# Kernel tuning notes

Hardware: AMD Instinct MI355X
Metric: run time of the kernel (lower is better)

## Reference

```python
import jax, jax.numpy as jnp
import numpy as np

N = 2048          # batch
T = 50            # max_num_visit
CODES = 40        # codes per visit
VOCAB = 527       # max_tokens for CategoryEncoding
MH = VOCAB - 1    # 526 after dropping column 0
AUX = 10          # aux_info feature dim
E = 256           # config.embedding_dim (LSTM units)


def setup_inputs() -> dict:
    key = jax.random.key(0)
    ks = jax.random.split(key, 10)
    code = jax.random.randint(ks[0], (N, T, CODES), 0, VOCAB, dtype=jnp.int32)
    aux_info = jax.random.normal(ks[1], (N, T, AUX), jnp.float32)
    length = jax.random.randint(ks[2], (N,), 1, T + 1, dtype=jnp.int32)

    def glorot(k, shape):
        fan = shape[0]
        return jax.random.normal(k, shape, jnp.float32) * (1.0 / np.sqrt(fan))

    W_lin = glorot(ks[3], (MH + AUX, E)); b_lin = jnp.zeros((E,), jnp.float32)
    K_lstm = glorot(ks[4], (E, 4 * E))
    R_lstm = glorot(ks[5], (E, 4 * E))
    b_lstm = jnp.zeros((4 * E,), jnp.float32)
    W0 = glorot(ks[6], (E, 256)); b0 = jnp.zeros((256,), jnp.float32)
    W1 = glorot(ks[7], (256, 256)); b1 = jnp.zeros((256,), jnp.float32)
    return dict(code=code, aux_info=aux_info, length=length, is_training=0,
                W_lin=W_lin, b_lin=b_lin, K_lstm=K_lstm, R_lstm=R_lstm,
                b_lstm=b_lstm, W0=W0, b0=b0, W1=W1, b1=b1)


def _multi_hot(code):
    # CategoryEncoding binary mode: presence indicator over vocab, drop col 0
    flat = code.reshape(N * T, CODES)
    mh = jnp.zeros((N * T, VOCAB), jnp.float32)
    mh = mh.at[jnp.arange(N * T)[:, None], flat].set(1.0)
    return mh[:, 1:].reshape(N, T, MH)


def _lstm(x, K, R, b):
    # Keras LSTM, gate order [i, f, g(c), o]; inference (dropout off)
    xz = jnp.einsum('nte,eh->nth', x, K) + b          # [N,T,4E]
    xz = jnp.transpose(xz, (1, 0, 2))                  # [T,N,4E]

    def step(carry, zt):
        h, c = carry
        z = zt + h @ R
        i, f, g, o = jnp.split(z, 4, axis=-1)
        c = jax.nn.sigmoid(f) * c + jax.nn.sigmoid(i) * jnp.tanh(g)
        h = jax.nn.sigmoid(o) * jnp.tanh(c)
        return (h, c), h

    h0 = jnp.zeros((N, E), jnp.float32)
    (_, _), hs = jax.lax.scan(step, (h0, h0), xz)
    return jnp.transpose(hs, (1, 0, 2))                # [N,T,E]


def reference(code, aux_info, length, is_training,
              W_lin, b_lin, K_lstm, R_lstm, b_lstm, W0, b0, W1, b1):
    mh = _multi_hot(code)                              # [N,T,526]
    x = jax.nn.relu(jnp.concatenate([mh, aux_info], axis=-1) @ W_lin + b_lin)
    h = _lstm(x, K_lstm, R_lstm, b_lstm)               # [N,T,E]
    x_last = h[jnp.arange(N), length - 1]              # gather_nd: last valid step
    fv = jax.nn.relu(x_last @ W0 + b0) @ W1 + b1
    fv = fv / jnp.sqrt(jnp.sum(fv ** 2, axis=-1, keepdims=True))
    return fv
```

## Files before the change

kernel.cpp:

```cpp
#include <hip/hip_runtime.h>
#include <hip/hip_bf16.h>
#include <math.h>
#include <stdint.h>

#define N_BATCH 2048
#define T_STEPS 50
#define NCODES  40
#define MH      526
#define AUXD    10
#define WLROWS  536
#define E_DIM   256
#define G_DIM   1024
#define TCHUNK  10
#define MBLK    64
#define NFUSED  (TCHUNK * 32)

typedef __attribute__((ext_vector_type(8))) short short8;
typedef __attribute__((ext_vector_type(4))) short short4v;
typedef __attribute__((ext_vector_type(4))) float f32x4;
typedef __attribute__((ext_vector_type(4))) int   i32x4;

__device__ __forceinline__ short f2bf(float f) {
    __hip_bfloat16 h = __float2bfloat16(f);
    return *reinterpret_cast<short*>(&h);
}
__device__ __forceinline__ float bf2f(unsigned short u) {
    return __uint_as_float(((unsigned int)u) << 16);
}
__device__ __forceinline__ float sigf(float x) {
    return 1.f / (1.f + __expf(-x));
}
__device__ __forceinline__ float tanhfast(float x) {
    return 2.f / (1.f + __expf(-2.f * x)) - 1.f;
}

__global__ __launch_bounds__(256) void k_zero(int* __restrict__ cnt)
{
    const int i = blockIdx.x * 256 + threadIdx.x;
    if (i < 3 * 64 * 32) cnt[i] = 0;
}

__global__ __launch_bounds__(256) void k_prep_wcoop(
    const float* __restrict__ R, short* __restrict__ Wcoop)
{
    const int gid  = blockIdx.x * 256 + threadIdx.x;
    const int fg   = gid >> 6, lane = gid & 63;
    const int p    = lane >> 4, lr = lane & 15;
    const int kk   = fg & 7;
    const int g    = (fg >> 3) & 3;
    const int w    = (fg >> 5) & 3;
    const int cs   = fg >> 7;
    const int n    = g * 256 + cs * 64 + w * 16 + lr;
    short* dst = Wcoop + (size_t)fg * 512 + lane * 8;
    #pragma unroll
    for (int j = 0; j < 8; ++j)
        dst[j] = f2bf(R[(size_t)(kk * 32 + p * 8 + j) * G_DIM + n]);
}

__global__ __launch_bounds__(256) void k_prep_wfk(
    const float* __restrict__ K, short* __restrict__ WfK)
{
    const int gid  = blockIdx.x * 256 + threadIdx.x;
    const int fg   = gid >> 6, lane = gid & 63;
    const int p    = lane >> 4, lr = lane & 15;
    const int kb   = fg >> 6;
    const int cb   = (fg >> 3) & 7;
    const int w    = fg & 7;
    const int n    = w * 128 + cb * 16 + lr;
    short* dst = WfK + (size_t)fg * 512 + lane * 8;
    #pragma unroll
    for (int j = 0; j < 8; ++j)
        dst[j] = f2bf(K[(size_t)(kb * 32 + p * 8 + j) * G_DIM + n]);
}

__global__ __launch_bounds__(256) void k_prep_wfl(
    const float* __restrict__ W_lin, short* __restrict__ WfL)
{
    const int gid  = blockIdx.x * 256 + threadIdx.x;
    const int fg   = gid >> 6, lane = gid & 63;
    const int p    = lane >> 4, lr = lane & 15;
    const int kk   = fg >> 4;
    const int cb   = (fg >> 3) & 1;
    const int w    = fg & 7;
    const int n    = w * 32 + cb * 16 + lr;
    short* dst = WfL + (size_t)fg * 512 + lane * 8;
    #pragma unroll
    for (int j = 0; j < 8; ++j) {
        const int k = kk * 32 + p * 8 + j;
        dst[j] = (k < WLROWS) ? f2bf(W_lin[(size_t)k * E_DIM + n]) : (short)0;
    }
}

__global__ __launch_bounds__(512, 1) void k_fused(
    const int* __restrict__ code, const float* __restrict__ aux,
    const short* __restrict__ WfL, const float* __restrict__ b_lin,
    const short* __restrict__ WfK, short* __restrict__ xzp, int t0f)
{
    const int tid  = threadIdx.x;
    const int w    = tid >> 6;
    const int lane = tid & 63;
    const int lr   = lane & 15;
    const int p    = lane >> 4;
    const int fid  = blockIdx.x;
    const int tl   = fid >> 5;
    const int ngg  = fid & 31;
    const int n0   = ngg * MBLK;
    const int t    = t0f + tl;
    const int ph8  = (fid >> 3) & 7;
    const int ph17 = (fid >> 3) % 17;

    __shared__ __align__(16) short oh[MBLK][552];
    __shared__ __align__(16) short xs[MBLK][264];

    for (int i = tid; i < (MBLK * 552) / 8; i += 512)
        ((int4*)&oh[0][0])[i] = (int4){0, 0, 0, 0};
    __syncthreads();

    for (int i = tid; i < MBLK * NCODES; i += 512) {
        const int r = i / NCODES;
        const int j = i - r * NCODES;
        const int c = code[((size_t)(n0 + r) * T_STEPS + t) * NCODES + j];
        if (c > 0) ((unsigned short*)&oh[0][0])[r * 552 + (c - 1)] = 0x3F80;
    }
    for (int i = tid; i < MBLK * AUXD; i += 512) {
        const int r = i / AUXD;
        const int a = i - r * AUXD;
        oh[r][MH + a] = f2bf(aux[((size_t)(n0 + r) * T_STEPS + t) * AUXD + a]);
    }
    __syncthreads();

    const short* wfl_thr = WfL + (size_t)w * 512 + lane * 8;
    const short* wfk_thr = WfK + (size_t)w * 512 + lane * 8;

    {
        f32x4 acc[4][2];
        #pragma unroll
        for (int rb = 0; rb < 4; ++rb)
            #pragma unroll
            for (int cb = 0; cb < 2; ++cb)
                acc[rb][cb] = (f32x4){0.f, 0.f, 0.f, 0.f};

        for (int kk = 0; kk < 17; ++kk) {
            int kx = kk + ph17; if (kx >= 17) kx -= 17;
            short8 a[4];
            #pragma unroll
            for (int rb = 0; rb < 4; ++rb)
                a[rb] = *(const short8*)&oh[rb * 16 + lr][kx * 32 + p * 8];
            #pragma unroll
            for (int cb = 0; cb < 2; ++cb) {
                short8 bf = *(const short8*)(wfl_thr + (size_t)(kx * 2 + cb) * 4096);
                #pragma unroll
                for (int rb = 0; rb < 4; ++rb)
                    acc[rb][cb] = __builtin_amdgcn_mfma_f32_16x16x32_bf16(
                        a[rb], bf, acc[rb][cb], 0, 0, 0);
            }
        }
        float bias[2];
        #pragma unroll
        for (int cb = 0; cb < 2; ++cb) bias[cb] = b_lin[w * 32 + cb * 16 + lr];
        #pragma unroll
        for (int rb = 0; rb < 4; ++rb)
            #pragma unroll
            for (int cb = 0; cb < 2; ++cb)
                #pragma unroll
                for (int rr = 0; rr < 4; ++rr)
                    xs[rb * 16 + p * 4 + rr][w * 32 + cb * 16 + lr] =
                        f2bf(fmaxf(acc[rb][cb][rr] + bias[cb], 0.f));
        __syncthreads();
    }

    #pragma unroll
    for (int half = 0; half < 2; ++half) {
        f32x4 acc[4][4];
        #pragma unroll
        for (int rb = 0; rb < 4; ++rb)
            #pragma unroll
            for (int c4 = 0; c4 < 4; ++c4)
                acc[rb][c4] = (f32x4){0.f, 0.f, 0.f, 0.f};

        for (int kb = 0; kb < 8; ++kb) {
            const int kx = (kb + ph8) & 7;
            short8 a[4];
            #pragma unroll
            for (int rb = 0; rb < 4; ++rb)
                a[rb] = *(const short8*)&xs[rb * 16 + lr][kx * 32 + p * 8];
            #pragma unroll
            for (int c4 = 0; c4 < 4; ++c4) {
                const int cb = half * 4 + c4;
                short8 bf = *(const short8*)(wfk_thr + (size_t)(kx * 8 + cb) * 4096);
                #pragma unroll
                for (int rb = 0; rb < 4; ++rb)
                    acc[rb][c4] = __builtin_amdgcn_mfma_f32_16x16x32_bf16(
                        a[rb], bf, acc[rb][c4], 0, 0, 0);
            }
        }
        #pragma unroll
        for (int rb = 0; rb < 4; ++rb) {
            const int rgg = ngg * 4 + rb;
            #pragma unroll
            for (int c4 = 0; c4 < 4; ++c4) {
                const int cb = half * 4 + c4;
                const int c0 = w * 128 + cb * 16;
                const int g  = c0 >> 8;
                const int wp = (c0 >> 5) & 7;
                const int eb = (c0 >> 4) & 1;
                const int j8 = eb * 4 + g;
                short4v v;
                #pragma unroll
                for (int rr = 0; rr < 4; ++rr) v[rr] = f2bf(acc[rb][c4][rr]);
                *(short4v*)(xzp +
                    (((size_t)rgg * TCHUNK + tl) * 64 + wp * 8 + j8) * 256 +
                    lane * 4) = v;
            }
        }
    }
}

__global__ __launch_bounds__(256, 1) void k_rcoop(
    const short* __restrict__ xz0, const short* __restrict__ xz1,
    const int* __restrict__ length,
    const short* __restrict__ Wcoop, const float* __restrict__ b,
    short* __restrict__ h_buf, float* __restrict__ c_state,
    float* __restrict__ xlast, int* __restrict__ flags,
    int t0, int nsteps)
{
    const int tid  = threadIdx.x;
    const int w    = tid >> 6;
    const int lane = tid & 63;
    const int lr   = lane & 15;
    const int p    = lane >> 4;
    const int cs   = blockIdx.x >> 6;
    const int rg   = blockIdx.x & 63;
    const int r0   = rg * 32;
    const int e    = cs * 64 + w * 16 + lr;

    __shared__ __align__(16) short h_o[32][64];
    __shared__ int s_len[32];
    if (tid < 32) s_len[tid] = length[r0 + tid];

    short8 bw[4][8];
    {
        const short* wb = Wcoop + ((size_t)((cs * 4 + w) * 4)) * 8 * 512 + lane * 8;
        #pragma unroll
        for (int g = 0; g < 4; ++g)
            #pragma unroll
            for (int kk = 0; kk < 8; ++kk)
                bw[g][kk] = *(const short8*)(wb + (size_t)(g * 8 + kk) * 512);
    }

    float bias[4];
    #pragma unroll
    for (int g = 0; g < 4; ++g) bias[g] = b[g * 256 + e];

    float creg[2][4];
    if (t0 == 0) {
        #pragma unroll
        for (int rf = 0; rf < 2; ++rf)
            #pragma unroll
            for (int rr = 0; rr < 4; ++rr) creg[rf][rr] = 0.f;
    } else {
        #pragma unroll
        for (int rf = 0; rf < 2; ++rf)
            #pragma unroll
            for (int rr = 0; rr < 4; ++rr)
                creg[rf][rr] = c_state[(size_t)(r0 + rf * 16 + p * 4 + rr) * E_DIM + e];
    }
    __syncthreads();

    int len_r[2][4];
    #pragma unroll
    for (int rf = 0; rf < 2; ++rf)
        #pragma unroll
        for (int rr = 0; rr < 4; ++rr)
            len_r[rf][rr] = s_len[rf * 16 + p * 4 + rr];

    const uint64_t slot_addr = (uint64_t)(uintptr_t)(flags + rg * 32 + cs);
    const uint64_t line_addr = (uint64_t)(uintptr_t)(flags + rg * 32);
    int bcnt = 0;

#define PEERS_BARRIER()                                                        \
    do {                                                                       \
        ++bcnt;                                                                \
        __syncthreads();               \
        if (tid == 0) {                                                        \
            asm volatile("global_store_dword %0, %1, off sc0 sc1"              \
                         :: "v"(slot_addr), "v"(bcnt) : "memory");             \
            i32x4 fv;                                                          \
            do {                                                               \
                asm volatile("global_load_dwordx4 %0, %1, off sc0 sc1\n\t"     \
                             "s_waitcnt vmcnt(0)"                              \
                             : "=v"(fv) : "v"(line_addr) : "memory");          \
            } while (fv[0] < bcnt || fv[1] < bcnt ||                           \
                     fv[2] < bcnt || fv[3] < bcnt);                            \
        }                                                                      \
        __syncthreads();                                                       \
    } while (0)

    if (t0 == 0) {
        const i32x4 z4 = {0, 0, 0, 0};
        const int row = tid >> 3, seg = tid & 7;
        const uint64_t dst = (uint64_t)(uintptr_t)(h_buf +
            (size_t)(r0 + row) * E_DIM + cs * 64 + seg * 8);
        asm volatile("global_store_dwordx4 %0, %1, off sc0 sc1"
                     :: "v"(dst), "v"(z4) : "memory");
        PEERS_BARRIER();
    }

    const short* hb0 = h_buf;
    const short* hb1 = h_buf + (size_t)N_BATCH * E_DIM;
    const size_t coloff = (size_t)((cs * 2 + (w >> 1)) * 8 + (w & 1) * 4) * 256 +
                          lane * 4;
    const size_t rowoff0 = (size_t)(2 * rg + 0) * TCHUNK * 16384;
    const size_t rowoff1 = (size_t)(2 * rg + 1) * TCHUNK * 16384;

#define XZ_BASE(T, RFOFF)                                                      \
    ((((((T) / TCHUNK) & 1) ? xz1 : xz0)) + (RFOFF) +                          \
     (size_t)((T) % TCHUNK) * 16384 + coloff)

    short4v xv[2][4];
    {
        const short* b0p = XZ_BASE(t0, rowoff0);
        const short* b1p = XZ_BASE(t0, rowoff1);
        #pragma unroll
        for (int g = 0; g < 4; ++g) {
            xv[0][g] = *(const short4v*)(b0p + g * 256);
            xv[1][g] = *(const short4v*)(b1p + g * 256);
        }
    }

    for (int s = 0; s < nsteps; ++s) {
        const int t = t0 + s;
        const short* hb_r = (t & 1) ? hb1 : hb0;

        short8 a[2][8];
        #pragma unroll
        for (int rf = 0; rf < 2; ++rf) {
            const uint64_t base = (uint64_t)(uintptr_t)(hb_r +
                (size_t)(r0 + rf * 16 + lr) * E_DIM + p * 8);
            asm volatile(
                "global_load_dwordx4 %0, %8, off sc0 sc1\n\t"
                "global_load_dwordx4 %1, %8, off offset:64 sc0 sc1\n\t"
                "global_load_dwordx4 %2, %8, off offset:128 sc0 sc1\n\t"
                "global_load_dwordx4 %3, %8, off offset:192 sc0 sc1\n\t"
                "global_load_dwordx4 %4, %8, off offset:256 sc0 sc1\n\t"
                "global_load_dwordx4 %5, %8, off offset:320 sc0 sc1\n\t"
                "global_load_dwordx4 %6, %8, off offset:384 sc0 sc1\n\t"
                "global_load_dwordx4 %7, %8, off offset:448 sc0 sc1"
                : "=&v"(a[rf][0]), "=&v"(a[rf][1]), "=&v"(a[rf][2]), "=&v"(a[rf][3]),
                  "=&v"(a[rf][4]), "=&v"(a[rf][5]), "=&v"(a[rf][6]), "=&v"(a[rf][7])
                : "v"(base));
        }

        f32x4 acc[2][4];
        #pragma unroll
        for (int rf = 0; rf < 2; ++rf)
            #pragma unroll
            for (int g = 0; g < 4; ++g)
                #pragma unroll
                for (int rr = 0; rr < 4; ++rr)
                    acc[rf][g][rr] = bf2f((unsigned short)xv[rf][g][rr]);

        asm volatile("s_waitcnt vmcnt(0)" ::: "memory");
        __builtin_amdgcn_sched_barrier(0);

        #pragma unroll
        for (int kk = 0; kk < 8; ++kk)
            #pragma unroll
            for (int g = 0; g < 4; ++g)
                #pragma unroll
                for (int rf = 0; rf < 2; ++rf)
                    acc[rf][g] = __builtin_amdgcn_mfma_f32_16x16x32_bf16(
                        a[rf][kk], bw[g][kk], acc[rf][g], 0, 0, 0);

        if (s + 1 < nsteps) {
            const short* b0p = XZ_BASE(t + 1, rowoff0);
            const short* b1p = XZ_BASE(t + 1, rowoff1);
            #pragma unroll
            for (int g = 0; g < 4; ++g) {
                xv[0][g] = *(const short4v*)(b0p + g * 256);
                xv[1][g] = *(const short4v*)(b1p + g * 256);
            }
        }

        #pragma unroll
        for (int rf = 0; rf < 2; ++rf) {
            #pragma unroll
            for (int rr = 0; rr < 4; ++rr) {
                float zi = acc[rf][0][rr] + bias[0];
                float zf = acc[rf][1][rr] + bias[1];
                float zg = acc[rf][2][rr] + bias[2];
                float zo = acc[rf][3][rr] + bias[3];
                float ig = sigf(zi), fg = sigf(zf);
                float gg = tanhfast(zg), og = sigf(zo);
                float cc = fg * creg[rf][rr] + ig * gg;
                float hh = og * tanhfast(cc);
                creg[rf][rr] = cc;
                h_o[rf * 16 + p * 4 + rr][w * 16 + lr] = f2bf(hh);
                const int row = r0 + rf * 16 + p * 4 + rr;
                if (t == len_r[rf][rr] - 1)
                    xlast[(size_t)row * E_DIM + e] = hh;
            }
        }
        __syncthreads();

        {
            short* hb_w = (short*)(((t + 1) & 1) ? hb1 : hb0);
            const int row = tid >> 3, seg = tid & 7;
            i32x4 v = *(const i32x4*)&h_o[row][seg * 8];
            const uint64_t dst = (uint64_t)(uintptr_t)(hb_w +
                (size_t)(r0 + row) * E_DIM + cs * 64 + seg * 8);
            asm volatile("global_store_dwordx4 %0, %1, off sc0 sc1"
                         :: "v"(dst), "v"(v) : "memory");
        }

        if (s + 1 < nsteps) PEERS_BARRIER();
    }

    #pragma unroll
    for (int rf = 0; rf < 2; ++rf)
        #pragma unroll
        for (int rr = 0; rr < 4; ++rr)
            c_state[(size_t)(r0 + rf * 16 + p * 4 + rr) * E_DIM + e] = creg[rf][rr];
#undef PEERS_BARRIER
#undef XZ_BASE
}

__global__ __launch_bounds__(256) void k_head(
    const float* __restrict__ xlast,
    const float* __restrict__ W0, const float* __restrict__ b0,
    const float* __restrict__ W1, const float* __restrict__ b1,
    float* __restrict__ out)
{
    const int n = blockIdx.x;
    const int j = threadIdx.x;

    __shared__ __align__(16) float xsh[E_DIM];
    __shared__ __align__(16) float y0[E_DIM];
    __shared__ float part[4];

    xsh[j] = xlast[(size_t)n * E_DIM + j];
    __syncthreads();

    float acc = b0[j];
    for (int k4 = 0; k4 < E_DIM; k4 += 4) {
        float4 xv = *reinterpret_cast<const float4*>(&xsh[k4]);
        #pragma unroll
        for (int kk = 0; kk < 4; ++kk)
            acc += (&xv.x)[kk] * W0[(size_t)(k4 + kk) * E_DIM + j];
    }
    y0[j] = fmaxf(acc, 0.f);
    __syncthreads();

    acc = b1[j];
    for (int k4 = 0; k4 < E_DIM; k4 += 4) {
        float4 yv = *reinterpret_cast<const float4*>(&y0[k4]);
        #pragma unroll
        for (int kk = 0; kk < 4; ++kk)
            acc += (&yv.x)[kk] * W1[(size_t)(k4 + kk) * E_DIM + j];
    }

    float sq = acc * acc;
    #pragma unroll
    for (int off = 32; off > 0; off >>= 1)
        sq += __shfl_xor(sq, off, 64);
    if ((j & 63) == 0) part[j >> 6] = sq;
    __syncthreads();
    float total = part[0] + part[1] + part[2] + part[3];

    out[(size_t)n * E_DIM + j] = acc * rsqrtf(total);
}

extern "C" void kernel_launch(void* const* d_in, const int* in_sizes, int n_in,
                              void* d_out, int out_size, void* d_ws, size_t ws_size,
                              hipStream_t stream) {
    const int*   code   = (const int*)  d_in[0];
    const float* aux    = (const float*)d_in[1];
    const int*   length = (const int*)  d_in[2];
    const float* W_lin  = (const float*)d_in[4];
    const float* b_lin  = (const float*)d_in[5];
    const float* K      = (const float*)d_in[6];
    const float* R      = (const float*)d_in[7];
    const float* b      = (const float*)d_in[8];
    const float* W0     = (const float*)d_in[9];
    const float* b0     = (const float*)d_in[10];
    const float* W1     = (const float*)d_in[11];
    const float* b1     = (const float*)d_in[12];
    float* out = (float*)d_out;

    char* ws = (char*)d_ws;
    short* Wcoop   = (short*)(ws + 0);
    short* WfK     = (short*)(ws + 524288);
    short* WfL     = (short*)(ws + 1048576);
    float* xlast   = (float*)(ws + 1327104);
    float* c_state = (float*)(ws + 3424256);
    short* h_buf   = (short*)(ws + 5521408);
    int*   flags   = (int*)  (ws + 7618560);
    short* xzp0    = (short*)(ws + 7643136);
    short* xzp1    = (short*)(ws + 49586176);

    k_zero      <<<24,  256, 0, stream>>>(flags);
    k_prep_wcoop<<<128, 256, 0, stream>>>(R, Wcoop);
    k_prep_wfk  <<<128, 256, 0, stream>>>(K, WfK);
    k_prep_wfl  <<<68,  256, 0, stream>>>(W_lin, WfL);

    k_fused<<<NFUSED, 512, 0, stream>>>(code, aux, WfL, b_lin, WfK, xzp0, 0);
    k_fused<<<NFUSED, 512, 0, stream>>>(code, aux, WfL, b_lin, WfK, xzp1, 10);
    k_rcoop<<<256, 256, 0, stream>>>(xzp0, xzp1, length, Wcoop, b, h_buf,
                                     c_state, xlast, flags + 0 * 2048, 0, 20);
    k_fused<<<NFUSED, 512, 0, stream>>>(code, aux, WfL, b_lin, WfK, xzp0, 20);
    k_fused<<<NFUSED, 512, 0, stream>>>(code, aux, WfL, b_lin, WfK, xzp1, 30);
    k_rcoop<<<256, 256, 0, stream>>>(xzp0, xzp1, length, Wcoop, b, h_buf,
                                     c_state, xlast, flags + 1 * 2048, 20, 20);
    k_fused<<<NFUSED, 512, 0, stream>>>(code, aux, WfL, b_lin, WfK, xzp0, 40);
    k_rcoop<<<256, 256, 0, stream>>>(xzp0, xzp1, length, Wcoop, b, h_buf,
                                     c_state, xlast, flags + 2 * 2048, 40, 10);

    k_head<<<N_BATCH, 256, 0, stream>>>(xlast, W0, b0, W1, b1, out);
}
```

Measured before the change: 478.8 us.

## Process 64 batch rows per recurrent block and stage h through LDS

The recurrent LSTM kernel now gives each block 64 batch rows instead of 32, halving the grid from 256 to 128 blocks. Each block still holds the same register-resident slice of R, so each weight load is reused over twice as many rows. The previous h state is loaded cooperatively with coalesced loads, rearranged into the MFMA operand layout in shared memory, and then read from LDS, replacing per-lane strided global loads. The trade-off is half as many blocks in flight (fewer CUs busy), more serial MFMA and gate work per block per step, and extra LDS traffic plus a __syncthreads.

```diff
diff --git a/kernel.cpp b/kernel.cpp
--- a/kernel.cpp
+++ b/kernel.cpp
@@ -37,7 +37,7 @@
 __global__ __launch_bounds__(256) void k_zero(int* __restrict__ cnt)
 {
     const int i = blockIdx.x * 256 + threadIdx.x;
-    if (i < 3 * 64 * 32) cnt[i] = 0;
+    if (i < 3 * 32 * 32) cnt[i] = 0;
 }
 
 __global__ __launch_bounds__(256) void k_prep_wcoop(
@@ -229,14 +229,15 @@
     const int lane = tid & 63;
     const int lr   = lane & 15;
     const int p    = lane >> 4;
-    const int cs   = blockIdx.x >> 6;
-    const int rg   = blockIdx.x & 63;
-    const int r0   = rg * 32;
+    const int cs   = blockIdx.x >> 5;
+    const int rgp  = blockIdx.x & 31;
+    const int r0   = rgp * 64;
     const int e    = cs * 64 + w * 16 + lr;
 
-    __shared__ __align__(16) short h_o[32][64];
-    __shared__ int s_len[32];
-    if (tid < 32) s_len[tid] = length[r0 + tid];
+    __shared__ __align__(16) short h_f[2][2][8][512];
+    __shared__ __align__(16) short h_o[2][32][64];
+    __shared__ int s_len[64];
+    if (tid < 64) s_len[tid] = length[r0 + tid];
 
     short8 bw[4][8];
     {
@@ -252,30 +253,37 @@
     #pragma unroll
     for (int g = 0; g < 4; ++g) bias[g] = b[g * 256 + e];
 
-    float creg[2][4];
+    float creg[2][2][4];
     if (t0 == 0) {
         #pragma unroll
+        for (int rg = 0; rg < 2; ++rg)
+            #pragma unroll
+            for (int rf = 0; rf < 2; ++rf)
+                #pragma unroll
+                for (int rr = 0; rr < 4; ++rr) creg[rg][rf][rr] = 0.f;
+    } else {
+        #pragma unroll
+        for (int rg = 0; rg < 2; ++rg)
+            #pragma unroll
+            for (int rf = 0; rf < 2; ++rf)
+                #pragma unroll
+                for (int rr = 0; rr < 4; ++rr)
+                    creg[rg][rf][rr] = c_state[
+                        (size_t)(r0 + rg * 32 + rf * 16 + p * 4 + rr) * E_DIM + e];
+    }
+    __syncthreads();
+
+    int len_r[2][2][4];
+    #pragma unroll
+    for (int rg = 0; rg < 2; ++rg)
+        #pragma unroll
         for (int rf = 0; rf < 2; ++rf)
             #pragma unroll
-            for (int rr = 0; rr < 4; ++rr) creg[rf][rr] = 0.f;
-    } else {
-        #pragma unroll
-        for (int rf = 0; rf < 2; ++rf)
-            #pragma unroll
             for (int rr = 0; rr < 4; ++rr)
-                creg[rf][rr] = c_state[(size_t)(r0 + rf * 16 + p * 4 + rr) * E_DIM + e];
-    }
-    __syncthreads();
-
-    int len_r[2][4];
-    #pragma unroll
-    for (int rf = 0; rf < 2; ++rf)
-        #pragma unroll
-        for (int rr = 0; rr < 4; ++rr)
-            len_r[rf][rr] = s_len[rf * 16 + p * 4 + rr];
-
-    const uint64_t slot_addr = (uint64_t)(uintptr_t)(flags + rg * 32 + cs);
-    const uint64_t line_addr = (uint64_t)(uintptr_t)(flags + rg * 32);
+                len_r[rg][rf][rr] = s_len[rg * 32 + rf * 16 + p * 4 + rr];
+
+    const uint64_t slot_addr = (uint64_t)(uintptr_t)(flags + rgp * 32 + cs);
+    const uint64_t line_addr = (uint64_t)(uintptr_t)(flags + rgp * 32);
     int bcnt = 0;
 
 #define PEERS_BARRIER()                                                        \
@@ -298,11 +306,15 @@
 
     if (t0 == 0) {
         const i32x4 z4 = {0, 0, 0, 0};
-        const int row = tid >> 3, seg = tid & 7;
-        const uint64_t dst = (uint64_t)(uintptr_t)(h_buf +
-            (size_t)(r0 + row) * E_DIM + cs * 64 + seg * 8);
-        asm volatile("global_store_dwordx4 %0, %1, off sc0 sc1"
-                     :: "v"(dst), "v"(z4) : "memory");
+        #pragma unroll
+        for (int rep = 0; rep < 2; ++rep) {
+            const int idx = tid + rep * 256;
+            const int row = idx >> 3, seg = idx & 7;
+            const uint64_t dst = (uint64_t)(uintptr_t)(h_buf +
+                (size_t)(r0 + row) * E_DIM + cs * 64 + seg * 8);
+            asm volatile("global_store_dwordx4 %0, %1, off sc0 sc1"
+                         :: "v"(dst), "v"(z4) : "memory");
+        }
         PEERS_BARRIER();
     }
 
@@ -310,117 +322,141 @@
     const short* hb1 = h_buf + (size_t)N_BATCH * E_DIM;
     const size_t coloff = (size_t)((cs * 2 + (w >> 1)) * 8 + (w & 1) * 4) * 256 +
                           lane * 4;
-    const size_t rowoff0 = (size_t)(2 * rg + 0) * TCHUNK * 16384;
-    const size_t rowoff1 = (size_t)(2 * rg + 1) * TCHUNK * 16384;
+    size_t rowoff[2][2];
+    #pragma unroll
+    for (int rg = 0; rg < 2; ++rg)
+        #pragma unroll
+        for (int rf = 0; rf < 2; ++rf)
+            rowoff[rg][rf] = (size_t)(rgp * 4 + rg * 2 + rf) * TCHUNK * 16384;
 
 #define XZ_BASE(T, RFOFF)                                                      \
     ((((((T) / TCHUNK) & 1) ? xz1 : xz0)) + (RFOFF) +                          \
      (size_t)((T) % TCHUNK) * 16384 + coloff)
 
-    short4v xv[2][4];
-    {
-        const short* b0p = XZ_BASE(t0, rowoff0);
-        const short* b1p = XZ_BASE(t0, rowoff1);
-        #pragma unroll
-        for (int g = 0; g < 4; ++g) {
-            xv[0][g] = *(const short4v*)(b0p + g * 256);
-            xv[1][g] = *(const short4v*)(b1p + g * 256);
-        }
-    }
+    short4v xv[2][2][4];
+    #pragma unroll
+    for (int rg = 0; rg < 2; ++rg)
+        #pragma unroll
+        for (int rf = 0; rf < 2; ++rf) {
+            const short* bp = XZ_BASE(t0, rowoff[rg][rf]);
+            #pragma unroll
+            for (int g = 0; g < 4; ++g)
+                xv[rg][rf][g] = *(const short4v*)(bp + g * 256);
+        }
 
     for (int s = 0; s < nsteps; ++s) {
         const int t = t0 + s;
         const short* hb_r = (t & 1) ? hb1 : hb0;
 
-        short8 a[2][8];
-        #pragma unroll
-        for (int rf = 0; rf < 2; ++rf) {
-            const uint64_t base = (uint64_t)(uintptr_t)(hb_r +
-                (size_t)(r0 + rf * 16 + lr) * E_DIM + p * 8);
-            asm volatile(
-                "global_load_dwordx4 %0, %8, off sc0 sc1\n\t"
-                "global_load_dwordx4 %1, %8, off offset:64 sc0 sc1\n\t"
-                "global_load_dwordx4 %2, %8, off offset:128 sc0 sc1\n\t"
-                "global_load_dwordx4 %3, %8, off offset:192 sc0 sc1\n\t"
-                "global_load_dwordx4 %4, %8, off offset:256 sc0 sc1\n\t"
-                "global_load_dwordx4 %5, %8, off offset:320 sc0 sc1\n\t"
-                "global_load_dwordx4 %6, %8, off offset:384 sc0 sc1\n\t"
-                "global_load_dwordx4 %7, %8, off offset:448 sc0 sc1"
-                : "=&v"(a[rf][0]), "=&v"(a[rf][1]), "=&v"(a[rf][2]), "=&v"(a[rf][3]),
-                  "=&v"(a[rf][4]), "=&v"(a[rf][5]), "=&v"(a[rf][6]), "=&v"(a[rf][7])
-                : "v"(base));
-        }
-
-        f32x4 acc[2][4];
-        #pragma unroll
-        for (int rf = 0; rf < 2; ++rf)
-            #pragma unroll
-            for (int g = 0; g < 4; ++g)
-                #pragma unroll
-                for (int rr = 0; rr < 4; ++rr)
-                    acc[rf][g][rr] = bf2f((unsigned short)xv[rf][g][rr]);
-
-        asm volatile("s_waitcnt vmcnt(0)" ::: "memory");
-        __builtin_amdgcn_sched_barrier(0);
-
-        #pragma unroll
-        for (int kk = 0; kk < 8; ++kk)
-            #pragma unroll
-            for (int g = 0; g < 4; ++g)
-                #pragma unroll
-                for (int rf = 0; rf < 2; ++rf)
-                    acc[rf][g] = __builtin_amdgcn_mfma_f32_16x16x32_bf16(
-                        a[rf][kk], bw[g][kk], acc[rf][g], 0, 0, 0);
+        {
+            short8 ld[8];
+            int dof[8];
+            #pragma unroll
+            for (int it = 0; it < 8; ++it) {
+                const int idx = tid + it * 256;
+                const int rg  = idx >> 10;
+                const int rem = idx & 1023;
+                const int row = rem >> 5;
+                const int ch  = rem & 31;
+                const uint64_t src = (uint64_t)(uintptr_t)(hb_r +
+                    (size_t)(r0 + rg * 32 + row) * E_DIM + ch * 8);
+                asm volatile("global_load_dwordx4 %0, %1, off sc0 sc1"
+                             : "=&v"(ld[it]) : "v"(src) : "memory");
+                dof[it] = ((rg * 2 + (row >> 4)) * 8 + (ch >> 2)) * 512 +
+                          ((ch & 3) * 16 + (row & 15)) * 8;
+            }
+            asm volatile("s_waitcnt vmcnt(0)" ::: "memory");
+            #pragma unroll
+            for (int it = 0; it < 8; ++it)
+                *(short8*)(&h_f[0][0][0][0] + dof[it]) = ld[it];
+        }
+        __syncthreads();
+
+        #pragma unroll
+        for (int rg = 0; rg < 2; ++rg) {
+            f32x4 acc[2][4];
+            #pragma unroll
+            for (int rf = 0; rf < 2; ++rf)
+                #pragma unroll
+                for (int g = 0; g < 4; ++g)
+                    #pragma unroll
+                    for (int rr = 0; rr < 4; ++rr)
+                        acc[rf][g][rr] = bf2f((unsigned short)xv[rg][rf][g][rr]);
+
+            #pragma unroll
+            for (int kk = 0; kk < 8; ++kk) {
+                short8 a0 = *(const short8*)&h_f[rg][0][kk][lane * 8];
+                short8 a1 = *(const short8*)&h_f[rg][1][kk][lane * 8];
+                #pragma unroll
+                for (int g = 0; g < 4; ++g) {
+                    acc[0][g] = __builtin_amdgcn_mfma_f32_16x16x32_bf16(
+                        a0, bw[g][kk], acc[0][g], 0, 0, 0);
+                    acc[1][g] = __builtin_amdgcn_mfma_f32_16x16x32_bf16(
+                        a1, bw[g][kk], acc[1][g], 0, 0, 0);
+                }
+            }
+
+            #pragma unroll
+            for (int rf = 0; rf < 2; ++rf) {
+                #pragma unroll
+                for (int rr = 0; rr < 4; ++rr) {
+                    float zi = acc[rf][0][rr] + bias[0];
+                    float zf = acc[rf][1][rr] + bias[1];
+                    float zg = acc[rf][2][rr] + bias[2];
+                    float zo = acc[rf][3][rr] + bias[3];
+                    float ig = sigf(zi), fg = sigf(zf);
+                    float gg = tanhfast(zg), og = sigf(zo);
+                    float cc = fg * creg[rg][rf][rr] + ig * gg;
+                    float hh = og * tanhfast(cc);
+                    creg[rg][rf][rr] = cc;
+                    h_o[rg][rf * 16 + p * 4 + rr][w * 16 + lr] = f2bf(hh);
+                    const int row = r0 + rg * 32 + rf * 16 + p * 4 + rr;
+                    if (t == len_r[rg][rf][rr] - 1)
+                        xlast[(size_t)row * E_DIM + e] = hh;
+                }
+            }
+        }
 
         if (s + 1 < nsteps) {
-            const short* b0p = XZ_BASE(t + 1, rowoff0);
-            const short* b1p = XZ_BASE(t + 1, rowoff1);
-            #pragma unroll
-            for (int g = 0; g < 4; ++g) {
-                xv[0][g] = *(const short4v*)(b0p + g * 256);
-                xv[1][g] = *(const short4v*)(b1p + g * 256);
-            }
-        }
-
-        #pragma unroll
-        for (int rf = 0; rf < 2; ++rf) {
-            #pragma unroll
-            for (int rr = 0; rr < 4; ++rr) {
-                float zi = acc[rf][0][rr] + bias[0];
-                float zf = acc[rf][1][rr] + bias[1];
-                float zg = acc[rf][2][rr] + bias[2];
-                float zo = acc[rf][3][rr] + bias[3];
-                float ig = sigf(zi), fg = sigf(zf);
-                float gg = tanhfast(zg), og = sigf(zo);
-                float cc = fg * creg[rf][rr] + ig * gg;
-                float hh = og * tanhfast(cc);
-                creg[rf][rr] = cc;
-                h_o[rf * 16 + p * 4 + rr][w * 16 + lr] = f2bf(hh);
-                const int row = r0 + rf * 16 + p * 4 + rr;
-                if (t == len_r[rf][rr] - 1)
-                    xlast[(size_t)row * E_DIM + e] = hh;
-            }
-        }
+            #pragma unroll
+            for (int rg = 0; rg < 2; ++rg)
+                #pragma unroll
+                for (int rf = 0; rf < 2; ++rf) {
+                    const short* bp = XZ_BASE(t + 1, rowoff[rg][rf]);
+                    #pragma unroll
+                    for (int g = 0; g < 4; ++g)
+                        xv[rg][rf][g] = *(const short4v*)(bp + g * 256);
+                }
+        }
+
         __syncthreads();
 
         {
             short* hb_w = (short*)(((t + 1) & 1) ? hb1 : hb0);
-            const int row = tid >> 3, seg = tid & 7;
-            i32x4 v = *(const i32x4*)&h_o[row][seg * 8];
-            const uint64_t dst = (uint64_t)(uintptr_t)(hb_w +
-                (size_t)(r0 + row) * E_DIM + cs * 64 + seg * 8);
-            asm volatile("global_store_dwordx4 %0, %1, off sc0 sc1"
-                         :: "v"(dst), "v"(v) : "memory");
+            #pragma unroll
+            for (int rep = 0; rep < 2; ++rep) {
+                const int idx = tid + rep * 256;
+                const int rg  = idx >> 8;
+                const int row = (idx & 255) >> 3, seg = idx & 7;
+                i32x4 v = *(const i32x4*)&h_o[rg][row][seg * 8];
+                const uint64_t dst = (uint64_t)(uintptr_t)(hb_w +
+                    (size_t)(r0 + rg * 32 + row) * E_DIM + cs * 64 + seg * 8);
+                asm volatile("global_store_dwordx4 %0, %1, off sc0 sc1"
+                             :: "v"(dst), "v"(v) : "memory");
+            }
         }
 
         if (s + 1 < nsteps) PEERS_BARRIER();
     }
 
     #pragma unroll
-    for (int rf = 0; rf < 2; ++rf)
-        #pragma unroll
-        for (int rr = 0; rr < 4; ++rr)
-            c_state[(size_t)(r0 + rf * 16 + p * 4 + rr) * E_DIM + e] = creg[rf][rr];
+    for (int rg = 0; rg < 2; ++rg)
+        #pragma unroll
+        for (int rf = 0; rf < 2; ++rf)
+            #pragma unroll
+            for (int rr = 0; rr < 4; ++rr)
+                c_state[(size_t)(r0 + rg * 32 + rf * 16 + p * 4 + rr) * E_DIM + e] =
+                    creg[rg][rf][rr];
 #undef PEERS_BARRIER
 #undef XZ_BASE
 }
@@ -495,25 +531,25 @@
     float* c_state = (float*)(ws + 3424256);
     short* h_buf   = (short*)(ws + 5521408);
     int*   flags   = (int*)  (ws + 7618560);
-    short* xzp0    = (short*)(ws + 7643136);
-    short* xzp1    = (short*)(ws + 49586176);
-
-    k_zero      <<<24,  256, 0, stream>>>(flags);
+    short* xzp0    = (short*)(ws + 7630848);
+    short* xzp1    = (short*)(ws + 49573888);
+
+    k_zero      <<<12,  256, 0, stream>>>(flags);
     k_prep_wcoop<<<128, 256, 0, stream>>>(R, Wcoop);
     k_prep_wfk  <<<128, 256, 0, stream>>>(K, WfK);
     k_prep_wfl  <<<68,  256, 0, stream>>>(W_lin, WfL);
 
     k_fused<<<NFUSED, 512, 0, stream>>>(code, aux, WfL, b_lin, WfK, xzp0, 0);
     k_fused<<<NFUSED, 512, 0, stream>>>(code, aux, WfL, b_lin, WfK, xzp1, 10);
-    k_rcoop<<<256, 256, 0, stream>>>(xzp0, xzp1, length, Wcoop, b, h_buf,
-                                     c_state, xlast, flags + 0 * 2048, 0, 20);
+    k_rcoop<<<128, 256, 0, stream>>>(xzp0, xzp1, length, Wcoop, b, h_buf,
+                                     c_state, xlast, flags + 0 * 1024, 0, 20);
     k_fused<<<NFUSED, 512, 0, stream>>>(code, aux, WfL, b_lin, WfK, xzp0, 20);
     k_fused<<<NFUSED, 512, 0, stream>>>(code, aux, WfL, b_lin, WfK, xzp1, 30);
-    k_rcoop<<<256, 256, 0, stream>>>(xzp0, xzp1, length, Wcoop, b, h_buf,
-                                     c_state, xlast, flags + 1 * 2048, 20, 20);
+    k_rcoop<<<128, 256, 0, stream>>>(xzp0, xzp1, length, Wcoop, b, h_buf,
+                                     c_state, xlast, flags + 1 * 1024, 20, 20);
     k_fused<<<NFUSED, 512, 0, stream>>>(code, aux, WfL, b_lin, WfK, xzp0, 40);
-    k_rcoop<<<256, 256, 0, stream>>>(xzp0, xzp1, length, Wcoop, b, h_buf,
-                                     c_state, xlast, flags + 2 * 2048, 40, 10);
+    k_rcoop<<<128, 256, 0, stream>>>(xzp0, xzp1, length, Wcoop, b, h_buf,
+                                     c_state, xlast, flags + 2 * 1024, 40, 10);
 
     k_head<<<N_BATCH, 256, 0, stream>>>(xlast, W0, b0, W1, b1, out);
 }
```

New measurement: 592.4 us. 23.7% more time.
